# Kernel tuning notes

Hardware: AMD Instinct MI355X
Metric: run time of the kernel (lower is better)

The kernel has to match this reference:

```python
import jax, jax.numpy as jnp
import numpy as np

N_NODES = 100000


def _gcn_layer(x, src, dst, W, b, num_nodes):
    # Linear transform first (PyG GCNConv applies Linear before propagate).
    h = x @ W.T  # [N, out]
    # Degree (with self loops already included in src/dst), computed on target.
    ones = jnp.ones(dst.shape[0], dtype=h.dtype)
    deg = jax.ops.segment_sum(ones, dst, num_segments=num_nodes)
    dinv = jnp.where(deg > 0, jax.lax.rsqrt(deg), 0.0)
    norm = dinv[src] * dinv[dst]  # [E]
    msg = h[src] * norm[:, None]  # gather + per-edge scale, [E, out]
    out = jax.ops.segment_sum(msg, dst, num_segments=num_nodes)
    return out + b


def setup_inputs() -> dict:
    key = jax.random.key(0)
    k1, k2, k3, k4, k5, k6 = jax.random.split(key, 6)
    d = 64
    x = jax.random.normal(k1, (N_NODES, d), dtype=jnp.float32)
    edge_index = jax.random.randint(k2, (2, 1600000), 0, N_NODES, dtype=jnp.int64)
    s = 1.0 / np.sqrt(d)
    W1 = jax.random.normal(k3, (d, d), dtype=jnp.float32) * s
    b1 = jax.random.normal(k4, (d,), dtype=jnp.float32) * 0.01
    W2 = jax.random.normal(k5, (d, d), dtype=jnp.float32) * s
    b2 = jax.random.normal(k6, (d,), dtype=jnp.float32) * 0.01
    return {"x": x, "edge_index": edge_index, "W1": W1, "b1": b1, "W2": W2, "b2": b2}


def reference(x, edge_index, W1, b1, W2, b2):
    n = x.shape[0]
    loop = jnp.arange(n, dtype=edge_index.dtype)
    src = jnp.concatenate([edge_index[0], loop])  # add self loops
    dst = jnp.concatenate([edge_index[1], loop])
    h = _gcn_layer(x, src, dst, W1, b1, n)
    out = _gcn_layer(h, src, dst, W2, b2, n)
    return out
```

## Files before the change

### kernel.cpp

```cpp
#include <hip/hip_runtime.h>
#include <hip/hip_fp16.h>


#define D 64
#define NPB 128
#define MAXB 784
#define CHUNK 4096
#define BT 512
#define CAP 3072

__global__ __launch_bounds__(BT) void build_scatter(const int* __restrict__ src,
                                                    const int* __restrict__ dst,
                                                    int* __restrict__ bcur,
                                                    int* __restrict__ entries0,
                                                    int nE, int B) {
    __shared__ int hist[MAXB];
    __shared__ int curs[MAXB];
    const int t = threadIdx.x;
    const int c = blockIdx.x;
    for (int b = t; b < B; b += BT) hist[b] = 0;
    __syncthreads();
    int e0 = c * CHUNK;
    int sv[CHUNK / BT], dv[CHUNK / BT];
#pragma unroll
    for (int i = 0; i < CHUNK / BT; ++i) {
        int e = e0 + i * BT + t;
        sv[i] = 0; dv[i] = -1;
        if (e < nE) {
            sv[i] = src[e];
            dv[i] = dst[e];
            atomicAdd(&hist[dv[i] >> 7], 1);
        }
    }
    __syncthreads();
    for (int b = t; b < B; b += BT) {
        int cnt = hist[b];
        int base = 0;
        if (cnt > 0) base = atomicAdd(&bcur[b], cnt);
        curs[b] = b * CAP + base;
    }
    __syncthreads();
#pragma unroll
    for (int i = 0; i < CHUNK / BT; ++i) {
        if (dv[i] >= 0) {
            int b = dv[i] >> 7;
            int pos = atomicAdd(&curs[b], 1);
            entries0[pos] = sv[i] | ((dv[i] & (NPB - 1)) << 17);
        }
    }
}

__device__ __forceinline__ void regroup_body(const int* __restrict__ entries0,
                                             int s0, int s1,
                                             int* __restrict__ off,
                                             int* __restrict__ deg,
                                             float* __restrict__ dinv,
                                             int* __restrict__ entries1,
                                             int* __restrict__ cursor, int N, int b,
                                             int* cnt, int* scn, int* cur, int* shb) {
    int t = threadIdx.x;
    if (t < NPB) cnt[t] = 0;
    if (t == 0) *shb = atomicAdd(cursor, s1 - s0);
    __syncthreads();
    for (int p = s0 + t; p < s1; p += 256)
        atomicAdd(&cnt[(entries0[p] >> 17) & (NPB - 1)], 1);
    __syncthreads();
    if (t < NPB) scn[t] = cnt[t];
    __syncthreads();
    for (int s = 1; s < NPB; s <<= 1) {
        int u = 0;
        if (t < NPB && t >= s) u = scn[t - s];
        __syncthreads();
        if (t < NPB) scn[t] += u;
        __syncthreads();
    }
    if (t < NPB) {
        int node = b * NPB + t;
        int c = cnt[t];
        int o = *shb + scn[t] - c;
        cur[t] = o;
        if (node < N) {
            off[node]  = o;
            deg[node]  = c;
            dinv[node] = rsqrtf((float)c + 1.0f);
        }
    }
    __syncthreads();
    for (int p = s0 + t; p < s1; p += 256) {
        int e = entries0[p];
        int pos = atomicAdd(&cur[(e >> 17) & (NPB - 1)], 1);
        entries1[pos] = e & 0x1FFFF;
    }
}

template <typename InT>
__device__ __forceinline__ void gemm_body(const InT* __restrict__ X,
                                          const float* __restrict__ W,
                                          const float* __restrict__ scale,
                                          __half* __restrict__ H, int N, int bx,
                                          float* xt, float* wt) {
    const int t = threadIdx.x;
    const int i0 = bx * 64;
#pragma unroll
    for (int r = 0; r < 16; ++r) {
        int idx = r * 256 + t;
        int j = idx >> 6, k = idx & 63;
        wt[k * 68 + j] = W[idx];
    }
#pragma unroll
    for (int r = 0; r < 16; ++r) {
        int idx = r * 256 + t;
        int i = idx >> 6, k = idx & 63;
        float v = 0.0f;
        if (i0 + i < N) {
            if constexpr (sizeof(InT) == 2)
                v = __half2float(((const __half*)X)[(size_t)(i0 + i) * D + k]);
            else
                v = ((const float*)X)[(size_t)(i0 + i) * D + k];
        }
        xt[k * 68 + i] = v;
    }
    __syncthreads();
    const int tn = (t & 15) * 4;
    const int tc = (t >> 4) * 4;
    float acc[4][4] = {};
#pragma unroll 8
    for (int k = 0; k < 64; ++k) {
        const float4 xa = *(const float4*)(xt + k * 68 + tn);
        const float4 wb = *(const float4*)(wt + k * 68 + tc);
        acc[0][0] += xa.x * wb.x; acc[0][1] += xa.x * wb.y; acc[0][2] += xa.x * wb.z; acc[0][3] += xa.x * wb.w;
        acc[1][0] += xa.y * wb.x; acc[1][1] += xa.y * wb.y; acc[1][2] += xa.y * wb.z; acc[1][3] += xa.y * wb.w;
        acc[2][0] += xa.z * wb.x; acc[2][1] += xa.z * wb.y; acc[2][2] += xa.z * wb.z; acc[2][3] += xa.z * wb.w;
        acc[3][0] += xa.w * wb.x; acc[3][1] += xa.w * wb.y; acc[3][2] += xa.w * wb.z; acc[3][3] += xa.w * wb.w;
    }
#pragma unroll
    for (int a = 0; a < 4; ++a) {
        int i = i0 + tn + a;
        if (i < N) {
            float sc = scale ? scale[i] : 1.0f;
            union { __half2 h2[2]; uint2 u2; } pk;
            pk.h2[0].x = __float2half_rn(acc[a][0] * sc);
            pk.h2[0].y = __float2half_rn(acc[a][1] * sc);
            pk.h2[1].x = __float2half_rn(acc[a][2] * sc);
            pk.h2[1].y = __float2half_rn(acc[a][3] * sc);
            *(uint2*)(&H[(size_t)i * D + tc]) = pk.u2;
        }
    }
}

template <typename InT>
__global__ __launch_bounds__(256) void gemm_xwt_h(const InT* __restrict__ X,
                                                  const float* __restrict__ W,
                                                  const float* __restrict__ scale,
                                                  __half* __restrict__ H, int N) {
    __shared__ float xt[64 * 68];
    __shared__ float wt[64 * 68];
    gemm_body<InT>(X, W, scale, H, N, blockIdx.x, xt, wt);
}

__global__ __launch_bounds__(256) void regroup_gemm1(const int* __restrict__ entries0,
                                                     const int* __restrict__ btot,
                                                     int* __restrict__ off,
                                                     int* __restrict__ deg,
                                                     float* __restrict__ dinv,
                                                     int* __restrict__ entries1,
                                                     int* __restrict__ cursor,
                                                     int N, int B,
                                                     const float* __restrict__ X,
                                                     const float* __restrict__ W1,
                                                     __half* __restrict__ Hh) {
    __shared__ float xt[64 * 68];
    __shared__ float wt[64 * 68];
    if ((int)blockIdx.x < B) {
        int b = blockIdx.x;
        int* cnt = (int*)xt;
        int* scn = cnt + NPB;
        int* cur = scn + NPB;
        int* shb = cur + NPB;
        regroup_body(entries0, b * CAP, b * CAP + btot[b], off, deg, dinv,
                     entries1, cursor, N, b, cnt, scn, cur, shb);
    } else {
        gemm_body<float>(X, W1, nullptr, Hh, N, (int)blockIdx.x - B, xt, wt);
    }
}

template <bool PRESCALED>
__device__ __forceinline__ float2 agg_node(const int* __restrict__ csr, int beg, int end,
                                           const __half2* __restrict__ H2,
                                           const float* __restrict__ dinv,
                                           float dd, int p2, int h) {
    float2 acc = make_float2(0.0f, 0.0f);
    int p = beg;
    for (; p + 16 <= end; p += 16) {
        int s[8];
#pragma unroll
        for (int i = 0; i < 8; ++i) s[i] = csr[p + 2 * i + h];
        __half2 g[8];
#pragma unroll
        for (int i = 0; i < 8; ++i) g[i] = H2[(size_t)s[i] * 32 + p2];
        if constexpr (PRESCALED) {
#pragma unroll
            for (int i = 0; i < 8; ++i) {
                float2 f = __half22float2(g[i]);
                acc.x += f.x; acc.y += f.y;
            }
        } else {
            float dv[8];
#pragma unroll
            for (int i = 0; i < 8; ++i) dv[i] = dinv[s[i]];
#pragma unroll
            for (int i = 0; i < 8; ++i) {
                float2 f = __half22float2(g[i]);
                float c = dv[i] * dd;
                acc.x += f.x * c; acc.y += f.y * c;
            }
        }
    }
    for (; p + 8 <= end; p += 8) {
        int s0v = csr[p + 0 + h], s1v = csr[p + 2 + h];
        int s2v = csr[p + 4 + h], s3v = csr[p + 6 + h];
        __half2 g0 = H2[(size_t)s0v * 32 + p2];
        __half2 g1 = H2[(size_t)s1v * 32 + p2];
        __half2 g2 = H2[(size_t)s2v * 32 + p2];
        __half2 g3 = H2[(size_t)s3v * 32 + p2];
        float2 f0 = __half22float2(g0), f1 = __half22float2(g1);
        float2 f2 = __half22float2(g2), f3 = __half22float2(g3);
        if constexpr (PRESCALED) {
            acc.x += f0.x + f1.x + f2.x + f3.x;
            acc.y += f0.y + f1.y + f2.y + f3.y;
        } else {
            float c0 = dinv[s0v] * dd, c1 = dinv[s1v] * dd;
            float c2 = dinv[s2v] * dd, c3 = dinv[s3v] * dd;
            acc.x += f0.x * c0; acc.y += f0.y * c0;
            acc.x += f1.x * c1; acc.y += f1.y * c1;
            acc.x += f2.x * c2; acc.y += f2.y * c2;
            acc.x += f3.x * c3; acc.y += f3.y * c3;
        }
    }
    for (; p + 2 <= end; p += 2) {
        int s0v = csr[p + h];
        __half2 g0 = H2[(size_t)s0v * 32 + p2];
        float2 f0 = __half22float2(g0);
        if constexpr (PRESCALED) {
            acc.x += f0.x; acc.y += f0.y;
        } else {
            float c0 = dinv[s0v] * dd;
            acc.x += f0.x * c0; acc.y += f0.y * c0;
        }
    }
    if (p < end && h == 0) {
        int s0v = csr[p];
        __half2 g0 = H2[(size_t)s0v * 32 + p2];
        float2 f0 = __half22float2(g0);
        if constexpr (PRESCALED) {
            acc.x += f0.x; acc.y += f0.y;
        } else {
            float c0 = dinv[s0v] * dd;
            acc.x += f0.x * c0; acc.y += f0.y * c0;
        }
    }
    return acc;
}

template <typename OutT, bool PRESCALED>
__global__ __launch_bounds__(256) void aggregate3(const int* __restrict__ csr,
                                                  const int* __restrict__ off,
                                                  const int* __restrict__ deg,
                                                  const float* __restrict__ dinv,
                                                  const __half* __restrict__ H,
                                                  const float* __restrict__ bias,
                                                  OutT* __restrict__ out, int N) {
    int node = blockIdx.x * 4 + (threadIdx.x >> 6);
    if (node >= N) return;
    int lane = threadIdx.x & 63;
    int p2 = lane & 31;
    int h  = lane >> 5;
    const __half2* H2 = (const __half2*)H;
    float dd = dinv[node];
    int beg = off[node];
    int end = beg + deg[node];
    float2 acc = agg_node<PRESCALED>(csr, beg, end, H2, dinv, dd, p2, h);
    acc.x += __shfl_xor(acc.x, 32);
    acc.y += __shfl_xor(acc.y, 32);
    if (h == 0) {
        float2 hs = __half22float2(H2[(size_t)node * 32 + p2]);
        float2 bv = ((const float2*)bias)[p2];
        float2 o;
        if constexpr (PRESCALED) {
            o.x = (acc.x + hs.x) * dd + bv.x;
            o.y = (acc.y + hs.y) * dd + bv.y;
        } else {
            float s = dd * dd;
            o.x = acc.x + bv.x + hs.x * s;
            o.y = acc.y + bv.y + hs.y * s;
        }
        if constexpr (sizeof(OutT) == 2) {
            ((__half2*)(out + (size_t)node * D))[p2] = __float22half2_rn(o);
        } else {
            ((float2*)(out + (size_t)node * D))[p2] = o;
        }
    }
}

__global__ __launch_bounds__(256) void deg_kernel(const int* __restrict__ dst,
                                                  int* __restrict__ deg, int nE) {
    int e = blockIdx.x * 256 + threadIdx.x;
    if (e < nE) atomicAdd(&deg[dst[e]], 1);
}

__global__ __launch_bounds__(256) void dinv_kernel(const int* __restrict__ deg,
                                                   float* __restrict__ dinv, int N) {
    int i = blockIdx.x * 256 + threadIdx.x;
    if (i < N) dinv[i] = rsqrtf((float)deg[i] + 1.0f);
}

__global__ __launch_bounds__(256) void gemm_xwt(const float* __restrict__ X,
                                                const float* __restrict__ W,
                                                float* __restrict__ H, int N) {
    __shared__ float xt[64 * 68];
    __shared__ float wt[64 * 68];
    const int t = threadIdx.x;
    const int i0 = blockIdx.x * 64;
#pragma unroll
    for (int r = 0; r < 16; ++r) {
        int idx = r * 256 + t;
        int j = idx >> 6, k = idx & 63;
        wt[k * 68 + j] = W[idx];
    }
#pragma unroll
    for (int r = 0; r < 16; ++r) {
        int idx = r * 256 + t;
        int i = idx >> 6, k = idx & 63;
        float v = 0.0f;
        if (i0 + i < N) v = X[(size_t)(i0 + i) * D + k];
        xt[k * 68 + i] = v;
    }
    __syncthreads();
    const int tn = (t & 15) * 4;
    const int tc = (t >> 4) * 4;
    float acc[4][4] = {};
#pragma unroll 8
    for (int k = 0; k < 64; ++k) {
        const float4 xa = *(const float4*)(xt + k * 68 + tn);
        const float4 wb = *(const float4*)(wt + k * 68 + tc);
        acc[0][0] += xa.x * wb.x; acc[0][1] += xa.x * wb.y; acc[0][2] += xa.x * wb.z; acc[0][3] += xa.x * wb.w;
        acc[1][0] += xa.y * wb.x; acc[1][1] += xa.y * wb.y; acc[1][2] += xa.y * wb.z; acc[1][3] += xa.y * wb.w;
        acc[2][0] += xa.z * wb.x; acc[2][1] += xa.z * wb.y; acc[2][2] += xa.z * wb.z; acc[2][3] += xa.z * wb.w;
        acc[3][0] += xa.w * wb.x; acc[3][1] += xa.w * wb.y; acc[3][2] += xa.w * wb.z; acc[3][3] += xa.w * wb.w;
    }
#pragma unroll
    for (int a = 0; a < 4; ++a) {
        int i = i0 + tn + a;
        if (i < N) {
            float4 o = make_float4(acc[a][0], acc[a][1], acc[a][2], acc[a][3]);
            *(float4*)(H + (size_t)i * D + tc) = o;
        }
    }
}

__global__ __launch_bounds__(256) void init_out(const float* __restrict__ H,
                                                const float* __restrict__ dinv,
                                                const float* __restrict__ b,
                                                float* __restrict__ out, int N) {
    int idx4 = blockIdx.x * 256 + threadIdx.x;
    if (idx4 >= N * 16) return;
    int i = idx4 >> 4;
    int jc = idx4 & 15;
    float di = dinv[i];
    float s = di * di;
    float4 h4 = ((const float4*)H)[idx4];
    float4 b4 = ((const float4*)b)[jc];
    ((float4*)out)[idx4] = make_float4(b4.x + h4.x * s, b4.y + h4.y * s,
                                       b4.z + h4.z * s, b4.w + h4.w * s);
}

__global__ __launch_bounds__(256) void edge_scatter(const int* __restrict__ src,
                                                    const int* __restrict__ dst,
                                                    const float* __restrict__ dinv,
                                                    const float* __restrict__ H,
                                                    float* __restrict__ out, int nE) {
    int tid = blockIdx.x * 256 + threadIdx.x;
    int e = tid >> 4;
    if (e >= nE) return;
    int l = tid & 15;
    int s = src[e];
    int d = dst[e];
    float c = dinv[s] * dinv[d];
    float4 v = ((const float4*)H)[s * 16 + l];
    float* o = out + (size_t)d * D + l * 4;
    unsafeAtomicAdd(o + 0, v.x * c);
    unsafeAtomicAdd(o + 1, v.y * c);
    unsafeAtomicAdd(o + 2, v.z * c);
    unsafeAtomicAdd(o + 3, v.w * c);
}

static inline size_t align_up(size_t v, size_t a) { return (v + a - 1) & ~(a - 1); }

extern "C" void kernel_launch(void* const* d_in, const int* in_sizes, int n_in,
                              void* d_out, int out_size, void* d_ws, size_t ws_size,
                              hipStream_t stream) {
    const float* x  = (const float*)d_in[0];
    const int*   ei = (const int*)d_in[1];
    const float* W1 = (const float*)d_in[2];
    const float* b1 = (const float*)d_in[3];
    const float* W2 = (const float*)d_in[4];
    const float* b2 = (const float*)d_in[5];
    float* out = (float*)d_out;

    const int N  = in_sizes[0] / D;
    const int nE = in_sizes[1] / 2;
    const int* srcp = ei;
    const int* dstv = ei + nE;

    const int B = (N + NPB - 1) / NPB;
    const int C = (nE + CHUNK - 1) / CHUNK;

    char* base_p = (char*)d_ws;

    int gb_n = (N + 255) / 256;
    int gb_g = (N + 63) / 64;
    int gb_e = (nE + 255) / 256;
    int gb_a = (N + 3) / 4;

    size_t o = 0;
    int* bcur   = (int*)(base_p + o);
    int* cursor = bcur + B;
    o = align_up(o + (size_t)(B + 1) * 4, 256);
    int* off    = (int*)(base_p + o);   o = align_up(o + (size_t)N * 4, 256);
    int* deg    = (int*)(base_p + o);   o = align_up(o + (size_t)N * 4, 256);
    float* dinv = (float*)(base_p + o); o = align_up(o + (size_t)N * 4, 256);
    int* entries1 = (int*)(base_p + o); o = align_up(o + (size_t)nE * 4, 256);
    size_t rE0 = (size_t)MAXB * CAP * 4;
    size_t rA1 = (size_t)N * D * 2;
    size_t rX  = rE0 > rA1 ? rE0 : rA1;
    int* entries0 = (int*)(base_p + o);
    __half* A1h   = (__half*)(base_p + o);
    o = align_up(o + rX, 256);
    __half* Hh    = (__half*)(base_p + o);
    size_t need1 = o + align_up((size_t)N * D * 2, 256);

    if (ws_size >= need1 && B <= MAXB - 2) {
        hipMemsetAsync(bcur, 0, (size_t)(B + 1) * 4, stream);
        build_scatter<<<C, BT, 0, stream>>>(srcp, dstv, bcur, entries0, nE, B);
        regroup_gemm1<<<B + gb_g, 256, 0, stream>>>(entries0, bcur, off, deg,
                                                    dinv, entries1, cursor,
                                                    N, B, x, W1, Hh);
        aggregate3<__half, false><<<gb_a, 256, 0, stream>>>(entries1, off, deg, dinv,
                                                            Hh, b1, A1h, N);
        gemm_xwt_h<__half><<<gb_g, 256, 0, stream>>>(A1h, W2, dinv, Hh, N);
        aggregate3<float, true><<<gb_a, 256, 0, stream>>>(entries1, off, deg, dinv,
                                                          Hh, b2, out, N);
    } else {
        size_t fo = 0;
        int* fdeg    = (int*)(base_p + fo);  fo = align_up(fo + (size_t)N * 4, 256);
        float* fdinv = (float*)(base_p + fo); fo = align_up(fo + (size_t)N * 4, 256);
        float* bufA  = (float*)(base_p + fo);
        hipMemsetAsync(fdeg, 0, (size_t)N * 4, stream);
        deg_kernel<<<gb_e, 256, 0, stream>>>(dstv, fdeg, nE);
        dinv_kernel<<<gb_n, 256, 0, stream>>>(fdeg, fdinv, N);
        int gb_i = (N * 16 + 255) / 256;
        int gb_e16 = (int)(((long long)nE * 16 + 255) / 256);
        gemm_xwt<<<gb_g, 256, 0, stream>>>(x, W1, bufA, N);
        init_out<<<gb_i, 256, 0, stream>>>(bufA, fdinv, b1, out, N);
        edge_scatter<<<gb_e16, 256, 0, stream>>>(srcp, dstv, fdinv, bufA, out, nE);
        gemm_xwt<<<gb_g, 256, 0, stream>>>(out, W2, bufA, N);
        init_out<<<gb_i, 256, 0, stream>>>(bufA, fdinv, b2, out, N);
        edge_scatter<<<gb_e16, 256, 0, stream>>>(srcp, dstv, fdinv, bufA, out, nE);
    }
}
```

Baseline: 274.5 us.

## Build CSR via global degree count, prefix alloc, and atomic scatter

Replaces the two-level bucketed scatter/regroup CSR build with three simpler passes: global atomic degree counting, a per-block scan that allocates unordered segment offsets (fused with the first GEMM), and a global atomic scatter of source indices. This removes the intermediate entries0 buffer and the bucket regrouping pass, at the cost of many contended global atomics and scattered writes with poor locality. Segment order across nodes is no longer contiguous by node id.

```diff
diff --git a/kernel.cpp b/kernel.cpp
--- a/kernel.cpp
+++ b/kernel.cpp
@@ -3,94 +3,22 @@
 
 
 #define D 64
-#define NPB 128
-#define MAXB 784
-#define CHUNK 4096
-#define BT 512
-#define CAP 3072
-
-__global__ __launch_bounds__(BT) void build_scatter(const int* __restrict__ src,
-                                                    const int* __restrict__ dst,
-                                                    int* __restrict__ bcur,
-                                                    int* __restrict__ entries0,
-                                                    int nE, int B) {
-    __shared__ int hist[MAXB];
-    __shared__ int curs[MAXB];
-    const int t = threadIdx.x;
-    const int c = blockIdx.x;
-    for (int b = t; b < B; b += BT) hist[b] = 0;
-    __syncthreads();
-    int e0 = c * CHUNK;
-    int sv[CHUNK / BT], dv[CHUNK / BT];
-#pragma unroll
-    for (int i = 0; i < CHUNK / BT; ++i) {
-        int e = e0 + i * BT + t;
-        sv[i] = 0; dv[i] = -1;
-        if (e < nE) {
-            sv[i] = src[e];
-            dv[i] = dst[e];
-            atomicAdd(&hist[dv[i] >> 7], 1);
-        }
-    }
-    __syncthreads();
-    for (int b = t; b < B; b += BT) {
-        int cnt = hist[b];
-        int base = 0;
-        if (cnt > 0) base = atomicAdd(&bcur[b], cnt);
-        curs[b] = b * CAP + base;
-    }
-    __syncthreads();
-#pragma unroll
-    for (int i = 0; i < CHUNK / BT; ++i) {
-        if (dv[i] >= 0) {
-            int b = dv[i] >> 7;
-            int pos = atomicAdd(&curs[b], 1);
-            entries0[pos] = sv[i] | ((dv[i] & (NPB - 1)) << 17);
-        }
-    }
-}
-
-__device__ __forceinline__ void regroup_body(const int* __restrict__ entries0,
-                                             int s0, int s1,
-                                             int* __restrict__ off,
-                                             int* __restrict__ deg,
-                                             float* __restrict__ dinv,
-                                             int* __restrict__ entries1,
-                                             int* __restrict__ cursor, int N, int b,
-                                             int* cnt, int* scn, int* cur, int* shb) {
-    int t = threadIdx.x;
-    if (t < NPB) cnt[t] = 0;
-    if (t == 0) *shb = atomicAdd(cursor, s1 - s0);
-    __syncthreads();
-    for (int p = s0 + t; p < s1; p += 256)
-        atomicAdd(&cnt[(entries0[p] >> 17) & (NPB - 1)], 1);
-    __syncthreads();
-    if (t < NPB) scn[t] = cnt[t];
-    __syncthreads();
-    for (int s = 1; s < NPB; s <<= 1) {
-        int u = 0;
-        if (t < NPB && t >= s) u = scn[t - s];
-        __syncthreads();
-        if (t < NPB) scn[t] += u;
-        __syncthreads();
-    }
-    if (t < NPB) {
-        int node = b * NPB + t;
-        int c = cnt[t];
-        int o = *shb + scn[t] - c;
-        cur[t] = o;
-        if (node < N) {
-            off[node]  = o;
-            deg[node]  = c;
-            dinv[node] = rsqrtf((float)c + 1.0f);
-        }
-    }
-    __syncthreads();
-    for (int p = s0 + t; p < s1; p += 256) {
-        int e = entries0[p];
-        int pos = atomicAdd(&cur[(e >> 17) & (NPB - 1)], 1);
-        entries1[pos] = e & 0x1FFFF;
-    }
+
+__global__ __launch_bounds__(256) void deg_count(const int* __restrict__ dst,
+                                                 int* __restrict__ deg, int nE) {
+    int tid = blockIdx.x * 256 + threadIdx.x;
+    int stride = gridDim.x * 256;
+    int n4 = nE >> 2;
+    const int4* d4 = (const int4*)dst;
+    for (int i = tid; i < n4; i += stride) {
+        int4 d = d4[i];
+        atomicAdd(&deg[d.x], 1);
+        atomicAdd(&deg[d.y], 1);
+        atomicAdd(&deg[d.z], 1);
+        atomicAdd(&deg[d.w], 1);
+    }
+    for (int e = (n4 << 2) + tid; e < nE; e += stride)
+        atomicAdd(&deg[dst[e]], 1);
 }
 
 template <typename InT>
@@ -158,29 +86,72 @@
     gemm_body<InT>(X, W, scale, H, N, blockIdx.x, xt, wt);
 }
 
-__global__ __launch_bounds__(256) void regroup_gemm1(const int* __restrict__ entries0,
-                                                     const int* __restrict__ btot,
-                                                     int* __restrict__ off,
-                                                     int* __restrict__ deg,
-                                                     float* __restrict__ dinv,
-                                                     int* __restrict__ entries1,
-                                                     int* __restrict__ cursor,
-                                                     int N, int B,
-                                                     const float* __restrict__ X,
-                                                     const float* __restrict__ W1,
-                                                     __half* __restrict__ Hh) {
+__global__ __launch_bounds__(256) void alloc_gemm1(const int* __restrict__ deg,
+                                                   int* __restrict__ off,
+                                                   float* __restrict__ dinv,
+                                                   int* __restrict__ cur,
+                                                   int* __restrict__ cursor,
+                                                   int N, int AB,
+                                                   const float* __restrict__ X,
+                                                   const float* __restrict__ W1,
+                                                   __half* __restrict__ Hh) {
     __shared__ float xt[64 * 68];
     __shared__ float wt[64 * 68];
-    if ((int)blockIdx.x < B) {
-        int b = blockIdx.x;
-        int* cnt = (int*)xt;
-        int* scn = cnt + NPB;
-        int* cur = scn + NPB;
-        int* shb = cur + NPB;
-        regroup_body(entries0, b * CAP, b * CAP + btot[b], off, deg, dinv,
-                     entries1, cursor, N, b, cnt, scn, cur, shb);
+    if ((int)blockIdx.x < AB) {
+        __shared__ int wtot[4];
+        __shared__ int bbase;
+        int t = threadIdx.x;
+        int node = blockIdx.x * 256 + t;
+        int v = (node < N) ? deg[node] : 0;
+        int lane = t & 63, w = t >> 6;
+        int x = v;
+#pragma unroll
+        for (int s = 1; s < 64; s <<= 1) {
+            int u = __shfl_up(x, s);
+            if (lane >= s) x += u;
+        }
+        if (lane == 63) wtot[w] = x;
+        __syncthreads();
+        int wbase = 0;
+        for (int i = 0; i < w; ++i) wbase += wtot[i];
+        if (t == 0) bbase = atomicAdd(cursor, wtot[0] + wtot[1] + wtot[2] + wtot[3]);
+        __syncthreads();
+        int excl = bbase + wbase + x - v;
+        if (node < N) {
+            off[node]  = excl;
+            cur[node]  = excl;
+            dinv[node] = rsqrtf((float)v + 1.0f);
+        }
     } else {
-        gemm_body<float>(X, W1, nullptr, Hh, N, (int)blockIdx.x - B, xt, wt);
+        gemm_body<float>(X, W1, nullptr, Hh, N, (int)blockIdx.x - AB, xt, wt);
+    }
+}
+
+__global__ __launch_bounds__(256) void scatter_kernel(const int* __restrict__ src,
+                                                      const int* __restrict__ dst,
+                                                      int* __restrict__ cur,
+                                                      int* __restrict__ entries1,
+                                                      int nE) {
+    int tid = blockIdx.x * 256 + threadIdx.x;
+    int stride = gridDim.x * 256;
+    int n4 = nE >> 2;
+    const int4* s4 = (const int4*)src;
+    const int4* d4 = (const int4*)dst;
+    for (int i = tid; i < n4; i += stride) {
+        int4 s = s4[i];
+        int4 d = d4[i];
+        int p0 = atomicAdd(&cur[d.x], 1);
+        int p1 = atomicAdd(&cur[d.y], 1);
+        int p2 = atomicAdd(&cur[d.z], 1);
+        int p3 = atomicAdd(&cur[d.w], 1);
+        entries1[p0] = s.x;
+        entries1[p1] = s.y;
+        entries1[p2] = s.z;
+        entries1[p3] = s.w;
+    }
+    for (int e = (n4 << 2) + tid; e < nE; e += stride) {
+        int pos = atomicAdd(&cur[dst[e]], 1);
+        entries1[pos] = src[e];
     }
 }
 
@@ -412,39 +383,32 @@
     const int* srcp = ei;
     const int* dstv = ei + nE;
 
-    const int B = (N + NPB - 1) / NPB;
-    const int C = (nE + CHUNK - 1) / CHUNK;
-
     char* base_p = (char*)d_ws;
 
     int gb_n = (N + 255) / 256;
     int gb_g = (N + 63) / 64;
     int gb_e = (nE + 255) / 256;
     int gb_a = (N + 3) / 4;
+    int AB   = (N + 255) / 256;
 
     size_t o = 0;
-    int* bcur   = (int*)(base_p + o);
-    int* cursor = bcur + B;
-    o = align_up(o + (size_t)(B + 1) * 4, 256);
+    int* deg    = (int*)(base_p + o);
+    int* cursor = deg + N;
+    o = align_up(o + (size_t)(N + 1) * 4, 256);
     int* off    = (int*)(base_p + o);   o = align_up(o + (size_t)N * 4, 256);
-    int* deg    = (int*)(base_p + o);   o = align_up(o + (size_t)N * 4, 256);
     float* dinv = (float*)(base_p + o); o = align_up(o + (size_t)N * 4, 256);
+    int* cur    = (int*)(base_p + o);   o = align_up(o + (size_t)N * 4, 256);
     int* entries1 = (int*)(base_p + o); o = align_up(o + (size_t)nE * 4, 256);
-    size_t rE0 = (size_t)MAXB * CAP * 4;
-    size_t rA1 = (size_t)N * D * 2;
-    size_t rX  = rE0 > rA1 ? rE0 : rA1;
-    int* entries0 = (int*)(base_p + o);
-    __half* A1h   = (__half*)(base_p + o);
-    o = align_up(o + rX, 256);
-    __half* Hh    = (__half*)(base_p + o);
+    __half* Hh  = (__half*)(base_p + o); o = align_up(o + (size_t)N * D * 2, 256);
+    __half* A1h = (__half*)(base_p + o);
     size_t need1 = o + align_up((size_t)N * D * 2, 256);
 
-    if (ws_size >= need1 && B <= MAXB - 2) {
-        hipMemsetAsync(bcur, 0, (size_t)(B + 1) * 4, stream);
-        build_scatter<<<C, BT, 0, stream>>>(srcp, dstv, bcur, entries0, nE, B);
-        regroup_gemm1<<<B + gb_g, 256, 0, stream>>>(entries0, bcur, off, deg,
-                                                    dinv, entries1, cursor,
-                                                    N, B, x, W1, Hh);
+    if (ws_size >= need1) {
+        hipMemsetAsync(deg, 0, (size_t)(N + 1) * 4, stream);
+        deg_count<<<1024, 256, 0, stream>>>(dstv, deg, nE);
+        alloc_gemm1<<<AB + gb_g, 256, 0, stream>>>(deg, off, dinv, cur, cursor,
+                                                   N, AB, x, W1, Hh);
+        scatter_kernel<<<1024, 256, 0, stream>>>(srcp, dstv, cur, entries1, nE);
         aggregate3<__half, false><<<gb_a, 256, 0, stream>>>(entries1, off, deg, dinv,
                                                             Hh, b1, A1h, N);
         gemm_xwt_h<__half><<<gb_g, 256, 0, stream>>>(A1h, W2, dinv, Hh, N);
```

After: 435.0 us. +58.4%, slower.

## Split bucket cursors into per-slice sub-buckets to reduce global atomic contention

Applied to the files above, without the earlier changes.

Each destination bucket is split into 8 sub-buckets, selected by chunk index, each with its own global cursor and a 512-entry capacity region. This spreads the global atomicAdd traffic during the scatter build across more addresses. In the regroup step each block gathers the 8 sub-buckets into a shared-memory staging buffer, so entries0 is read from global memory only once, and the second pass reads from LDS. The risks are overflow if any sub-bucket exceeds 512 entries (about 256 expected) and shared-memory staging capacity, which is limited to the xt buffer of 4352 ints.

```diff
diff --git a/kernel.cpp b/kernel.cpp
--- a/kernel.cpp
+++ b/kernel.cpp
@@ -7,7 +7,8 @@
 #define MAXB 784
 #define CHUNK 4096
 #define BT 512
-#define CAP 3072
+#define SL 8
+#define CAP8 512
 
 __global__ __launch_bounds__(BT) void build_scatter(const int* __restrict__ src,
                                                     const int* __restrict__ dst,
@@ -18,6 +19,7 @@
     __shared__ int curs[MAXB];
     const int t = threadIdx.x;
     const int c = blockIdx.x;
+    const int x = c & (SL - 1);
     for (int b = t; b < B; b += BT) hist[b] = 0;
     __syncthreads();
     int e0 = c * CHUNK;
@@ -36,8 +38,8 @@
     for (int b = t; b < B; b += BT) {
         int cnt = hist[b];
         int base = 0;
-        if (cnt > 0) base = atomicAdd(&bcur[b], cnt);
-        curs[b] = b * CAP + base;
+        if (cnt > 0) base = atomicAdd(&bcur[b * SL + x], cnt);
+        curs[b] = (b * SL + x) * CAP8 + base;
     }
     __syncthreads();
 #pragma unroll
@@ -51,19 +53,30 @@
 }
 
 __device__ __forceinline__ void regroup_body(const int* __restrict__ entries0,
-                                             int s0, int s1,
+                                             const int* __restrict__ btot,
                                              int* __restrict__ off,
                                              int* __restrict__ deg,
                                              float* __restrict__ dinv,
                                              int* __restrict__ entries1,
                                              int* __restrict__ cursor, int N, int b,
-                                             int* cnt, int* scn, int* cur, int* shb) {
+                                             int* stage, int* cnt, int* scn,
+                                             int* cur, int* shb) {
     int t = threadIdx.x;
     if (t < NPB) cnt[t] = 0;
-    if (t == 0) *shb = atomicAdd(cursor, s1 - s0);
-    __syncthreads();
-    for (int p = s0 + t; p < s1; p += 256)
-        atomicAdd(&cnt[(entries0[p] >> 17) & (NPB - 1)], 1);
+    __syncthreads();
+    int tot = 0;
+#pragma unroll
+    for (int x = 0; x < SL; ++x) {
+        int n_x = btot[b * SL + x];
+        int base = (b * SL + x) * CAP8;
+        for (int p = t; p < n_x; p += 256) {
+            int e = entries0[base + p];
+            stage[tot + p] = e;
+            atomicAdd(&cnt[(e >> 17) & (NPB - 1)], 1);
+        }
+        tot += n_x;
+    }
+    if (t == 0) *shb = atomicAdd(cursor, tot);
     __syncthreads();
     if (t < NPB) scn[t] = cnt[t];
     __syncthreads();
@@ -86,8 +99,8 @@
         }
     }
     __syncthreads();
-    for (int p = s0 + t; p < s1; p += 256) {
-        int e = entries0[p];
+    for (int p = t; p < tot; p += 256) {
+        int e = stage[p];
         int pos = atomicAdd(&cur[(e >> 17) & (NPB - 1)], 1);
         entries1[pos] = e & 0x1FFFF;
     }
@@ -173,12 +186,13 @@
     __shared__ float wt[64 * 68];
     if ((int)blockIdx.x < B) {
         int b = blockIdx.x;
-        int* cnt = (int*)xt;
+        int* stage = (int*)xt;
+        int* cnt = (int*)wt;
         int* scn = cnt + NPB;
         int* cur = scn + NPB;
         int* shb = cur + NPB;
-        regroup_body(entries0, b * CAP, b * CAP + btot[b], off, deg, dinv,
-                     entries1, cursor, N, b, cnt, scn, cur, shb);
+        regroup_body(entries0, btot, off, deg, dinv, entries1, cursor, N, b,
+                     stage, cnt, scn, cur, shb);
     } else {
         gemm_body<float>(X, W1, nullptr, Hh, N, (int)blockIdx.x - B, xt, wt);
     }
@@ -424,13 +438,13 @@
 
     size_t o = 0;
     int* bcur   = (int*)(base_p + o);
-    int* cursor = bcur + B;
-    o = align_up(o + (size_t)(B + 1) * 4, 256);
+    int* cursor = bcur + B * SL;
+    o = align_up(o + (size_t)(B * SL + 1) * 4, 256);
     int* off    = (int*)(base_p + o);   o = align_up(o + (size_t)N * 4, 256);
     int* deg    = (int*)(base_p + o);   o = align_up(o + (size_t)N * 4, 256);
     float* dinv = (float*)(base_p + o); o = align_up(o + (size_t)N * 4, 256);
     int* entries1 = (int*)(base_p + o); o = align_up(o + (size_t)nE * 4, 256);
-    size_t rE0 = (size_t)MAXB * CAP * 4;
+    size_t rE0 = (size_t)MAXB * SL * CAP8 * 4;
     size_t rA1 = (size_t)N * D * 2;
     size_t rX  = rE0 > rA1 ? rE0 : rA1;
     int* entries0 = (int*)(base_p + o);
@@ -440,7 +454,7 @@
     size_t need1 = o + align_up((size_t)N * D * 2, 256);
 
     if (ws_size >= need1 && B <= MAXB - 2) {
-        hipMemsetAsync(bcur, 0, (size_t)(B + 1) * 4, stream);
+        hipMemsetAsync(bcur, 0, (size_t)(B * SL + 1) * 4, stream);
         build_scatter<<<C, BT, 0, stream>>>(srcp, dstv, bcur, entries0, nE, B);
         regroup_gemm1<<<B + gb_g, 256, 0, stream>>>(entries0, bcur, off, deg,
                                                     dinv, entries1, cursor,
```

New measurement: 274.8 us. Within noise of the previous version (+0.1%).
